# Kernel optimization log

Hardware: AMD Instinct MI355X
Metric: run time of the kernel (lower is better)

Reference implementation:

```python
import jax, jax.numpy as jnp
import numpy as np

N_CLUSTERS = 512
TEMPERATURE = 0.1


def setup_inputs() -> dict:
    key = jax.random.key(0)
    k1, k2 = jax.random.split(key)
    x = jax.random.normal(k1, (32, 1024, 256), dtype=jnp.float32)
    centroids = jax.random.normal(k2, (N_CLUSTERS, 256), dtype=jnp.float32)
    return {"x": x, "centroids": centroids}


def reference(x, centroids):
    # Flatten non-cluster axes into a sample axis: [N, D]
    B, S, D = x.shape
    xf = x.reshape(-1, D)  # [N, D]
    x_sq = jnp.sum(xf * xf, axis=-1, keepdims=True)           # [N, 1]
    c_sq = jnp.sum(centroids * centroids, axis=-1)             # [K]
    cross = jnp.einsum('nd,kd->nk', xf, centroids)             # [N, K]
    dists = x_sq - 2.0 * cross + c_sq[None, :]                 # [N, K]
    # Temperature-scaled soft assignments
    assignments = jax.nn.softmax(-dists / TEMPERATURE, axis=-1)  # [N, K]
    # Restore leading (non-feature) dims, append cluster axis
    return assignments.reshape(B, S, N_CLUSTERS)
```

## Files before the change

### kernel.cpp

```cpp
#include <hip/hip_runtime.h>

#define NROWS 32768
#define KC 512
#define DDIM 256
#define BM 64
#define BK 16
#define KCH (DDIM / BK)
#define CHUNK_USH (KC * BK)

typedef __attribute__((ext_vector_type(8)))  short bf16x8;
typedef __attribute__((ext_vector_type(16))) float f32x16;

union U8 { unsigned short u[8]; bf16x8 v; };

__device__ __forceinline__ unsigned short f2bf(float f) {
    union { float f; unsigned int u; } a; a.f = f;
    unsigned int r = a.u + 0x7fffu + ((a.u >> 16) & 1u);
    return (unsigned short)(r >> 16);
}
__device__ __forceinline__ float bf2f(unsigned short h) {
    union { unsigned int u; float f; } a; a.u = ((unsigned int)h) << 16;
    return a.f;
}
__device__ __forceinline__ void ld16(const void* g, void* l) {
    __builtin_amdgcn_global_load_lds(
        (const __attribute__((address_space(1))) unsigned int*)g,
        (__attribute__((address_space(3))) unsigned int*)l, 16, 0, 0);
}

__global__ __launch_bounds__(64) void prep_c(const float* __restrict__ c,
                                             unsigned short* __restrict__ bhi,
                                             unsigned short* __restrict__ blo,
                                             float* __restrict__ csq10) {
    const int n = blockIdx.x, lane = threadIdx.x;
    const int d0 = lane * 4;
    float4 v = ((const float4*)(c + (size_t)n * DDIM))[lane];
    float vv[4] = {v.x, v.y, v.z, v.w};
    unsigned short hh[4], ll[4];
    float ssq = 0.f;
    #pragma unroll
    for (int i = 0; i < 4; ++i) {
        ssq += vv[i] * vv[i];
        hh[i] = f2bf(vv[i]);
        ll[i] = f2bf(vv[i] - bf2f(hh[i]));
    }
    #pragma unroll
    for (int off = 32; off; off >>= 1) ssq += __shfl_xor(ssq, off);
    if (lane == 0) csq10[n] = 10.f * ssq;
    const int ks = d0 >> 4;
    const int h  = (d0 >> 3) & 1;
    const int j0 = d0 & 7;
    const int c5 = n & 31, tile = n >> 5;
    const int p  = (2 * c5 + h) ^ ((c5 >> 2) & 1);
    const size_t dst = (size_t)ks * CHUNK_USH + tile * 512 + p * 8 + j0;
    *(ushort4*)(bhi + dst) = make_ushort4(hh[0], hh[1], hh[2], hh[3]);
    *(ushort4*)(blo + dst) = make_ushort4(ll[0], ll[1], ll[2], ll[3]);
}

union SmemU {
    struct { unsigned short Bh[2][CHUNK_USH], Bl[2][CHUNK_USH]; } k;
    float lbuf[16 * 516];
};

__global__ __launch_bounds__(256, 2) void kmeans_mfma(
    const float* __restrict__ x, const unsigned short* __restrict__ bhi,
    const unsigned short* __restrict__ blo, const float* __restrict__ csq10,
    float* __restrict__ out) {
    __shared__ __align__(16) SmemU sm;
    __shared__ float  red0[2][BM], red1[2][BM];
    __shared__ float2 MI[BM];

    const int tid  = threadIdx.x;
    const int w    = tid >> 6, lane = tid & 63;
    const int wm   = w >> 1, wn = w & 1;
    const int c5   = lane & 31, h = lane >> 5;
    const int row0 = blockIdx.x * BM;

    f32x16 acc[8];
    #pragma unroll
    for (int t = 0; t < 8; ++t)
        #pragma unroll
        for (int r = 0; r < 16; ++r) acc[t][r] = 0.f;

    const float* xrow = x + (size_t)(row0 + wm * 32 + c5) * DDIM + h * 8;
    const int bRd    = ((2 * c5 + h) ^ ((c5 >> 2) & 1)) * 8;
    const int dmaOff = (w * 4) * 512;

    #pragma unroll
    for (int j = 0; j < 4; ++j) {
        const int o = dmaOff + j * 512;
        ld16(bhi + o + lane * 8, &sm.k.Bh[0][o]);
        ld16(blo + o + lane * 8, &sm.k.Bl[0][o]);
    }
    float4 a0 = *(const float4*)xrow;
    float4 a1 = *(const float4*)(xrow + 4);
    __syncthreads();

    for (int ks = 0; ks < KCH; ++ks) {
        const int pp = ks & 1;
        float4 n0, n1;
        if (ks < KCH - 1) {
            const size_t cb = (size_t)(ks + 1) * CHUNK_USH;
            #pragma unroll
            for (int j = 0; j < 4; ++j) {
                const int o = dmaOff + j * 512;
                ld16(bhi + cb + o + lane * 8, &sm.k.Bh[1 - pp][o]);
                ld16(blo + cb + o + lane * 8, &sm.k.Bl[1 - pp][o]);
            }
            n0 = *(const float4*)(xrow + (ks + 1) * BK);
            n1 = *(const float4*)(xrow + (ks + 1) * BK + 4);
        }
        bf16x8 ah, al;
        {
            float v8[8] = {a0.x, a0.y, a0.z, a0.w, a1.x, a1.y, a1.z, a1.w};
            U8 H, L;
            #pragma unroll
            for (int i = 0; i < 8; ++i) {
                H.u[i] = f2bf(v8[i]);
                L.u[i] = f2bf(v8[i] - bf2f(H.u[i]));
            }
            ah = H.v; al = L.v;
        }
        #pragma unroll
        for (int t = 0; t < 8; ++t) {
            const int bo = (wn * 8 + t) * 512 + bRd;
            bf16x8 bh = *(const bf16x8*)&sm.k.Bh[pp][bo];
            bf16x8 bl = *(const bf16x8*)&sm.k.Bl[pp][bo];
            acc[t] = __builtin_amdgcn_mfma_f32_32x32x16_bf16(ah, bh, acc[t], 0, 0, 0);
            acc[t] = __builtin_amdgcn_mfma_f32_32x32x16_bf16(ah, bl, acc[t], 0, 0, 0);
            acc[t] = __builtin_amdgcn_mfma_f32_32x32x16_bf16(al, bh, acc[t], 0, 0, 0);
        }
        a0 = n0; a1 = n1;
        __syncthreads();
    }

    float csqv[8];
    #pragma unroll
    for (int t = 0; t < 8; ++t) csqv[t] = csq10[wn * 256 + t * 32 + c5];

    #pragma unroll
    for (int r = 0; r < 16; ++r) {
        float pm = -1e30f;
        #pragma unroll
        for (int t = 0; t < 8; ++t) pm = fmaxf(pm, 20.f * acc[t][r] - csqv[t]);
        #pragma unroll
        for (int off = 1; off < 32; off <<= 1) pm = fmaxf(pm, __shfl_xor(pm, off));
        if (c5 == 0) red0[wn][wm * 32 + (r & 3) + 8 * (r >> 2) + 4 * h] = pm;
    }
    __syncthreads();
    #pragma unroll
    for (int r = 0; r < 16; ++r) {
        const int row = wm * 32 + (r & 3) + 8 * (r >> 2) + 4 * h;
        const float Mf = fmaxf(red0[0][row], red0[1][row]);
        float ps = 0.f;
        #pragma unroll
        for (int t = 0; t < 8; ++t) ps += __expf(20.f * acc[t][r] - csqv[t] - Mf);
        #pragma unroll
        for (int off = 1; off < 32; off <<= 1) ps += __shfl_xor(ps, off);
        if (c5 == 0) red1[wn][row] = ps;
    }
    __syncthreads();
    if (tid < BM) {
        const float Mf = fmaxf(red0[0][tid], red0[1][tid]);
        const float Sf = red1[0][tid] + red1[1][tid];
        MI[tid] = make_float2(Mf, 1.f / Sf);
    }
    __syncthreads();

    #pragma unroll
    for (int p = 0; p < 4; ++p) {
        if (wm == (p >> 1)) {
            #pragma unroll
            for (int i = 0; i < 8; ++i) {
                const int    rr  = (p & 1) * 8 + i;
                const int    lr  = (i & 3) + 8 * (i >> 2) + 4 * h;
                const float2 mi  = MI[p * 16 + lr];
                #pragma unroll
                for (int t = 0; t < 8; ++t)
                    sm.lbuf[lr * 516 + wn * 256 + t * 32 + c5] =
                        __expf(20.f * acc[t][rr] - csqv[t] - mi.x) * mi.y;
            }
        }
        __syncthreads();
        #pragma unroll
        for (int j = 0; j < 8; ++j) {
            const int f    = j * 256 + tid;
            const int lrow = f >> 7;
            const int c4   = f & 127;
            float4    v    = *(const float4*)&sm.lbuf[lrow * 516 + c4 * 4];
            *(float4*)(out + (size_t)(row0 + p * 16 + lrow) * KC + c4 * 4) = v;
        }
        __syncthreads();
    }
}

extern "C" void kernel_launch(void* const* d_in, const int* in_sizes, int n_in,
                              void* d_out, int out_size, void* d_ws, size_t ws_size,
                              hipStream_t stream) {
    const float* x   = (const float*)d_in[0];
    const float* c   = (const float*)d_in[1];
    float*       out = (float*)d_out;

    unsigned short* bhi   = (unsigned short*)d_ws;
    unsigned short* blo   = bhi + (size_t)KCH * CHUNK_USH;
    float*          csq10 = (float*)(blo + (size_t)KCH * CHUNK_USH);

    prep_c<<<KC, 64, 0, stream>>>(c, bhi, blo, csq10);
    kmeans_mfma<<<NROWS / BM, 256, 0, stream>>>(x, bhi, blo, csq10, out);
}
```

Measured before the change: 123.0 us.

## Load centroid MFMA fragments directly from global memory instead of LDS staging

Removes the double-buffered LDS staging of the bf16 hi/lo centroid chunks and has each wave load its B fragments straight from global memory into registers. The prep kernel now writes the layout in the exact per-lane fragment order, without the XOR swizzle. This cuts LDS footprint and LDS traffic, which may allow more resident blocks. In exchange it gives up the prefetch of the next chunk, so global load latency is exposed each iteration, and the centroid data is read once per wave instead of once per block. The loop also keeps a __syncthreads that now has no shared data to protect.

```diff
diff --git a/kernel.cpp b/kernel.cpp
--- a/kernel.cpp
+++ b/kernel.cpp
@@ -22,11 +22,6 @@
     union { unsigned int u; float f; } a; a.u = ((unsigned int)h) << 16;
     return a.f;
 }
-__device__ __forceinline__ void ld16(const void* g, void* l) {
-    __builtin_amdgcn_global_load_lds(
-        (const __attribute__((address_space(1))) unsigned int*)g,
-        (__attribute__((address_space(3))) unsigned int*)l, 16, 0, 0);
-}
 
 __global__ __launch_bounds__(64) void prep_c(const float* __restrict__ c,
                                              unsigned short* __restrict__ bhi,
@@ -50,23 +45,17 @@
     const int ks = d0 >> 4;
     const int h  = (d0 >> 3) & 1;
     const int j0 = d0 & 7;
-    const int c5 = n & 31, tile = n >> 5;
-    const int p  = (2 * c5 + h) ^ ((c5 >> 2) & 1);
-    const size_t dst = (size_t)ks * CHUNK_USH + tile * 512 + p * 8 + j0;
+    const size_t dst = (size_t)ks * CHUNK_USH + (n >> 5) * 512 +
+                       (h * 32 + (n & 31)) * 8 + j0;
     *(ushort4*)(bhi + dst) = make_ushort4(hh[0], hh[1], hh[2], hh[3]);
     *(ushort4*)(blo + dst) = make_ushort4(ll[0], ll[1], ll[2], ll[3]);
 }
-
-union SmemU {
-    struct { unsigned short Bh[2][CHUNK_USH], Bl[2][CHUNK_USH]; } k;
-    float lbuf[16 * 516];
-};
 
 __global__ __launch_bounds__(256, 2) void kmeans_mfma(
     const float* __restrict__ x, const unsigned short* __restrict__ bhi,
     const unsigned short* __restrict__ blo, const float* __restrict__ csq10,
     float* __restrict__ out) {
-    __shared__ __align__(16) SmemU sm;
+    __shared__ float  lbuf[16 * 516];
     __shared__ float  red0[2][BM], red1[2][BM];
     __shared__ float2 MI[BM];
 
@@ -83,33 +72,20 @@
         for (int r = 0; r < 16; ++r) acc[t][r] = 0.f;
 
     const float* xrow = x + (size_t)(row0 + wm * 32 + c5) * DDIM + h * 8;
-    const int bRd    = ((2 * c5 + h) ^ ((c5 >> 2) & 1)) * 8;
-    const int dmaOff = (w * 4) * 512;
-
-    #pragma unroll
-    for (int j = 0; j < 4; ++j) {
-        const int o = dmaOff + j * 512;
-        ld16(bhi + o + lane * 8, &sm.k.Bh[0][o]);
-        ld16(blo + o + lane * 8, &sm.k.Bl[0][o]);
-    }
-    float4 a0 = *(const float4*)xrow;
-    float4 a1 = *(const float4*)(xrow + 4);
-    __syncthreads();
+    const unsigned short* bhB = bhi + (wn * 8) * 512 + lane * 8;
+    const unsigned short* blB = blo + (wn * 8) * 512 + lane * 8;
 
     for (int ks = 0; ks < KCH; ++ks) {
-        const int pp = ks & 1;
-        float4 n0, n1;
-        if (ks < KCH - 1) {
-            const size_t cb = (size_t)(ks + 1) * CHUNK_USH;
-            #pragma unroll
-            for (int j = 0; j < 4; ++j) {
-                const int o = dmaOff + j * 512;
-                ld16(bhi + cb + o + lane * 8, &sm.k.Bh[1 - pp][o]);
-                ld16(blo + cb + o + lane * 8, &sm.k.Bl[1 - pp][o]);
-            }
-            n0 = *(const float4*)(xrow + (ks + 1) * BK);
-            n1 = *(const float4*)(xrow + (ks + 1) * BK + 4);
-        }
+        const size_t cb = (size_t)ks * CHUNK_USH;
+        bf16x8 bh[8], bl[8];
+        #pragma unroll
+        for (int t = 0; t < 8; ++t) bh[t] = *(const bf16x8*)(bhB + cb + t * 512);
+        #pragma unroll
+        for (int t = 0; t < 8; ++t) bl[t] = *(const bf16x8*)(blB + cb + t * 512);
+        float4 a0 = *(const float4*)(xrow + ks * BK);
+        float4 a1 = *(const float4*)(xrow + ks * BK + 4);
+        __syncthreads();
+
         bf16x8 ah, al;
         {
             float v8[8] = {a0.x, a0.y, a0.z, a0.w, a1.x, a1.y, a1.z, a1.w};
@@ -123,15 +99,10 @@
         }
         #pragma unroll
         for (int t = 0; t < 8; ++t) {
-            const int bo = (wn * 8 + t) * 512 + bRd;
-            bf16x8 bh = *(const bf16x8*)&sm.k.Bh[pp][bo];
-            bf16x8 bl = *(const bf16x8*)&sm.k.Bl[pp][bo];
-            acc[t] = __builtin_amdgcn_mfma_f32_32x32x16_bf16(ah, bh, acc[t], 0, 0, 0);
-            acc[t] = __builtin_amdgcn_mfma_f32_32x32x16_bf16(ah, bl, acc[t], 0, 0, 0);
-            acc[t] = __builtin_amdgcn_mfma_f32_32x32x16_bf16(al, bh, acc[t], 0, 0, 0);
+            acc[t] = __builtin_amdgcn_mfma_f32_32x32x16_bf16(ah, bh[t], acc[t], 0, 0, 0);
+            acc[t] = __builtin_amdgcn_mfma_f32_32x32x16_bf16(ah, bl[t], acc[t], 0, 0, 0);
+            acc[t] = __builtin_amdgcn_mfma_f32_32x32x16_bf16(al, bh[t], acc[t], 0, 0, 0);
         }
-        a0 = n0; a1 = n1;
-        __syncthreads();
     }
 
     float csqv[8];
@@ -150,8 +121,8 @@
     __syncthreads();
     #pragma unroll
     for (int r = 0; r < 16; ++r) {
-        const int row = wm * 32 + (r & 3) + 8 * (r >> 2) + 4 * h;
-        const float Mf = fmaxf(red0[0][row], red0[1][row]);
+        const int   row = wm * 32 + (r & 3) + 8 * (r >> 2) + 4 * h;
+        const float Mf  = fmaxf(red0[0][row], red0[1][row]);
         float ps = 0.f;
         #pragma unroll
         for (int t = 0; t < 8; ++t) ps += __expf(20.f * acc[t][r] - csqv[t] - Mf);
@@ -172,12 +143,12 @@
         if (wm == (p >> 1)) {
             #pragma unroll
             for (int i = 0; i < 8; ++i) {
-                const int    rr  = (p & 1) * 8 + i;
-                const int    lr  = (i & 3) + 8 * (i >> 2) + 4 * h;
-                const float2 mi  = MI[p * 16 + lr];
+                const int    rr = (p & 1) * 8 + i;
+                const int    lr = (i & 3) + 8 * (i >> 2) + 4 * h;
+                const float2 mi = MI[p * 16 + lr];
                 #pragma unroll
                 for (int t = 0; t < 8; ++t)
-                    sm.lbuf[lr * 516 + wn * 256 + t * 32 + c5] =
+                    lbuf[lr * 516 + wn * 256 + t * 32 + c5] =
                         __expf(20.f * acc[t][rr] - csqv[t] - mi.x) * mi.y;
             }
         }
@@ -187,7 +158,7 @@
             const int f    = j * 256 + tid;
             const int lrow = f >> 7;
             const int c4   = f & 127;
-            float4    v    = *(const float4*)&sm.lbuf[lrow * 516 + c4 * 4];
+            float4    v    = *(const float4*)&lbuf[lrow * 516 + c4 * 4];
             *(float4*)(out + (size_t)(row0 + p * 16 + lrow) * KC + c4 * 4) = v;
         }
         __syncthreads();
```

Result: no change. 124.8 us (+1.4%).
